# Kernel optimization log

Hardware: AMD Instinct MI355X
Metric: run time of the kernel (lower is better)

Reference implementation:

```python
import jax, jax.numpy as jnp
import numpy as np

WEIGHT_THRESH = 0.0
EPS = 1e-5


def setup_inputs() -> dict:
    key = jax.random.key(0)
    k1, k2, k3 = jax.random.split(key, 3)
    B, N = 8192, 1024
    src_points = jax.random.normal(k1, (B, N, 3), dtype=jnp.float32)
    tgt_points = jax.random.normal(k2, (B, N, 3), dtype=jnp.float32)
    weights = jax.random.uniform(k3, (B, N), dtype=jnp.float32)
    return {"src_points": src_points, "tgt_points": tgt_points, "weights": weights}


def reference(src_points, tgt_points, weights):
    # Threshold and normalize weights: (B, N)
    w = jnp.where(weights < WEIGHT_THRESH, jnp.zeros_like(weights), weights)
    w = w / (jnp.sum(w, axis=1, keepdims=True) + EPS)
    w3 = w[..., None]  # (B, N, 1)

    # Weighted centroids: (B, 1, 3)
    src_centroid = jnp.sum(src_points * w3, axis=1, keepdims=True)
    tgt_centroid = jnp.sum(tgt_points * w3, axis=1, keepdims=True)

    src_c = src_points - src_centroid
    tgt_c = tgt_points - tgt_centroid

    # Weighted covariance H = src_c^T @ (w * tgt_c): (B, 3, 3)
    H = jnp.einsum('bnc,bnd->bcd', src_c, w3 * tgt_c)

    # torch.svd returns U, S, V with H = U S V^T; jnp returns U, S, Vh
    U, _, Vh = jnp.linalg.svd(H)
    V = jnp.swapaxes(Vh, -1, -2)
    Ut = jnp.swapaxes(U, -1, -2)

    # Reflection correction: E = diag(1, 1, sign(det(V @ Ut)))
    s = jnp.sign(jnp.linalg.det(jnp.matmul(V, Ut)))  # (B,)
    d = jnp.stack([jnp.ones_like(s), jnp.ones_like(s), s], axis=-1)  # (B, 3)
    R = jnp.matmul(V, Ut * d[..., None])  # V @ diag(d) @ Ut, (B, 3, 3)

    # Translation: t = tgt_centroid - R @ src_centroid, (B, 3)
    t = tgt_centroid[:, 0, :] - jnp.einsum('bij,bj->bi', R, src_centroid[:, 0, :])

    # Assemble 4x4 transform
    B = src_points.shape[0]
    top = jnp.concatenate([R, t[..., None]], axis=-1)  # (B, 3, 4)
    bottom = jnp.broadcast_to(
        jnp.array([[0.0, 0.0, 0.0, 1.0]], dtype=R.dtype), (B, 1, 4)
    )
    transform = jnp.concatenate([top, bottom], axis=1)  # (B, 4, 4)
    return transform
```

## Files before the change

kernel.cpp:

```cpp
#include <hip/hip_runtime.h>
#include <math.h>

#define TPB 256
#define NPTS 1024

template<int P, int Q, int R>
__device__ __forceinline__ void jrot(float a[3][3], float V[3][3]) {
  float apq = a[P][Q];
  if (fabsf(apq) < 1e-30f) return;
  float theta = (a[Q][Q] - a[P][P]) / (2.0f * apq);
  float t = copysignf(1.0f, theta) / (fabsf(theta) + sqrtf(theta * theta + 1.0f));
  float c = 1.0f / sqrtf(t * t + 1.0f);
  float s = t * c;
  float app = a[P][P], aqq = a[Q][Q];
  a[P][P] = app - t * apq;
  a[Q][Q] = aqq + t * apq;
  a[P][Q] = 0.0f; a[Q][P] = 0.0f;
  float arp = a[R][P], arq = a[R][Q];
  a[R][P] = c * arp - s * arq; a[P][R] = a[R][P];
  a[R][Q] = s * arp + c * arq; a[Q][R] = a[R][Q];
#pragma unroll
  for (int i = 0; i < 3; ++i) {
    float vip = V[i][P], viq = V[i][Q];
    V[i][P] = c * vip - s * viq;
    V[i][Q] = s * vip + c * viq;
  }
}

#define CSWAP(I, J)                                                        \
  if (ev[I] < ev[J]) {                                                     \
    float e_ = ev[I]; ev[I] = ev[J]; ev[J] = e_;                           \
    _Pragma("unroll")                                                      \
    for (int r2_ = 0; r2_ < 3; ++r2_) {                                    \
      float v_ = V[r2_][I]; V[r2_][I] = V[r2_][J]; V[r2_][J] = v_;         \
    }                                                                      \
  }

__device__ __forceinline__ void svd_tail_write(const float r[16], float* o) {
  const float S = r[0];
  const float inv = 1.0f / (S + 1e-5f);
  const float sc[3] = {r[1] * inv, r[2] * inv, r[3] * inv};
  const float tc[3] = {r[4] * inv, r[5] * inv, r[6] * inv};
  const float f = 2.0f - S * inv;

  float H[3][3];
#pragma unroll
  for (int c = 0; c < 3; ++c)
#pragma unroll
    for (int d = 0; d < 3; ++d)
      H[c][d] = r[7 + 3 * c + d] * inv - sc[c] * tc[d] * f;

  float Bm[3][3];
#pragma unroll
  for (int i = 0; i < 3; ++i)
#pragma unroll
    for (int j = 0; j < 3; ++j)
      Bm[i][j] = H[0][i] * H[0][j] + H[1][i] * H[1][j] + H[2][i] * H[2][j];

  float V[3][3] = {{1, 0, 0}, {0, 1, 0}, {0, 0, 1}};
  for (int sweep = 0; sweep < 8; ++sweep) {
    jrot<0, 1, 2>(Bm, V);
    jrot<0, 2, 1>(Bm, V);
    jrot<1, 2, 0>(Bm, V);
  }
  float ev[3] = {Bm[0][0], Bm[1][1], Bm[2][2]};
  CSWAP(0, 1)
  CSWAP(1, 2)
  CSWAP(0, 1)

  float U[3][3];
  float w0[3], w1[3];
#pragma unroll
  for (int i = 0; i < 3; ++i)
    w0[i] = H[i][0] * V[0][0] + H[i][1] * V[1][0] + H[i][2] * V[2][0];
  float n0 = sqrtf(w0[0] * w0[0] + w0[1] * w0[1] + w0[2] * w0[2]);
  float in0 = (n0 > 1e-20f) ? 1.0f / n0 : 0.0f;
#pragma unroll
  for (int i = 0; i < 3; ++i) U[i][0] = w0[i] * in0;

#pragma unroll
  for (int i = 0; i < 3; ++i)
    w1[i] = H[i][0] * V[0][1] + H[i][1] * V[1][1] + H[i][2] * V[2][1];
  float d01 = U[0][0] * w1[0] + U[1][0] * w1[1] + U[2][0] * w1[2];
#pragma unroll
  for (int i = 0; i < 3; ++i) w1[i] -= d01 * U[i][0];
  float n1 = sqrtf(w1[0] * w1[0] + w1[1] * w1[1] + w1[2] * w1[2]);
  float in1 = (n1 > 1e-20f) ? 1.0f / n1 : 0.0f;
#pragma unroll
  for (int i = 0; i < 3; ++i) U[i][1] = w1[i] * in1;

  U[0][2] = U[1][0] * U[2][1] - U[2][0] * U[1][1];
  U[1][2] = U[2][0] * U[0][1] - U[0][0] * U[2][1];
  U[2][2] = U[0][0] * U[1][1] - U[1][0] * U[0][1];

  float detV = V[0][0] * (V[1][1] * V[2][2] - V[1][2] * V[2][1]) -
               V[0][1] * (V[1][0] * V[2][2] - V[1][2] * V[2][0]) +
               V[0][2] * (V[1][0] * V[2][1] - V[1][1] * V[2][0]);
  float s3 = (detV >= 0.0f) ? 1.0f : -1.0f;

  float R[3][3];
#pragma unroll
  for (int i = 0; i < 3; ++i)
#pragma unroll
    for (int j = 0; j < 3; ++j)
      R[i][j] = V[i][0] * U[j][0] + V[i][1] * U[j][1] + s3 * V[i][2] * U[j][2];

  float tr[3];
#pragma unroll
  for (int i = 0; i < 3; ++i)
    tr[i] = tc[i] - (R[i][0] * sc[0] + R[i][1] * sc[1] + R[i][2] * sc[2]);

  float4* o4 = (float4*)o;
  o4[0] = make_float4(R[0][0], R[0][1], R[0][2], tr[0]);
  o4[1] = make_float4(R[1][0], R[1][1], R[1][2], tr[1]);
  o4[2] = make_float4(R[2][0], R[2][1], R[2][2], tr[2]);
  o4[3] = make_float4(0.0f, 0.0f, 0.0f, 1.0f);
}

__global__ __launch_bounds__(TPB) void wproc_fused(
    const float* __restrict__ src, const float* __restrict__ tgt,
    const float* __restrict__ wts, float* __restrict__ out) {
  const int b = blockIdx.x;
  const int t = threadIdx.x;
  const int lane = t & 63, wave = t >> 6;

  __shared__ float4 sh_src[NPTS * 3 / 4];
  __shared__ float4 sh_tgt[NPTS * 3 / 4];
  __shared__ float sh_fin[4][17];
  __shared__ float sh_r[16];
  float(*sh_part)[20] = (float(*)[20])sh_src;

  const float4* g_src = (const float4*)(src + (size_t)b * (NPTS * 3));
  const float4* g_tgt = (const float4*)(tgt + (size_t)b * (NPTS * 3));
  const float* g_w = wts + (size_t)b * NPTS;

#pragma unroll
  for (int i = 0; i < 3; ++i) {
    sh_src[t + i * TPB] = g_src[t + i * TPB];
    sh_tgt[t + i * TPB] = g_tgt[t + i * TPB];
  }
  const float wv0 = g_w[t], wv1 = g_w[t + 256], wv2 = g_w[t + 512],
              wv3 = g_w[t + 768];
  __syncthreads();

  const float* ss = (const float*)sh_src;
  const float* st = (const float*)sh_tgt;

  float acc[16];
#pragma unroll
  for (int k = 0; k < 16; ++k) acc[k] = 0.0f;

  const float wreg[4] = {wv0, wv1, wv2, wv3};
#pragma unroll
  for (int i = 0; i < 4; ++i) {
    const int p = t + i * TPB;
    float wv = fmaxf(wreg[i], 0.0f);
    const float sx = ss[3 * p + 0], sy = ss[3 * p + 1], sz = ss[3 * p + 2];
    const float tx = st[3 * p + 0], ty = st[3 * p + 1], tz = st[3 * p + 2];
    const float wsx = wv * sx, wsy = wv * sy, wsz = wv * sz;
    acc[0] += wv;
    acc[1] += wsx;      acc[2] += wsy;      acc[3] += wsz;
    acc[4] += wv * tx;  acc[5] += wv * ty;  acc[6] += wv * tz;
    acc[7]  += wsx * tx; acc[8]  += wsx * ty; acc[9]  += wsx * tz;
    acc[10] += wsy * tx; acc[11] += wsy * ty; acc[12] += wsy * tz;
    acc[13] += wsz * tx; acc[14] += wsz * ty; acc[15] += wsz * tz;
  }

#pragma unroll
  for (int k = 0; k < 16; ++k) acc[k] += __shfl_down(acc[k], 32, 64);
#pragma unroll
  for (int k = 0; k < 16; ++k) acc[k] += __shfl_down(acc[k], 16, 64);

  __syncthreads();

  if (lane < 16) {
    float4* pr = (float4*)&sh_part[wave * 16 + lane][0];
    pr[0] = make_float4(acc[0], acc[1], acc[2], acc[3]);
    pr[1] = make_float4(acc[4], acc[5], acc[6], acc[7]);
    pr[2] = make_float4(acc[8], acc[9], acc[10], acc[11]);
    pr[3] = make_float4(acc[12], acc[13], acc[14], acc[15]);
  }
  __syncthreads();

  if (t < 64) {
    const int k = t & 15, g = t >> 4;
    float s = 0.0f;
#pragma unroll
    for (int j = 0; j < 16; ++j) s += sh_part[g * 16 + j][k];
    sh_fin[g][k] = s;
  }
  __syncthreads();

  if (t < 16)
    sh_r[t] = sh_fin[0][t] + sh_fin[1][t] + sh_fin[2][t] + sh_fin[3][t];
  __syncthreads();

  if (t != 0) return;
  float r[16];
#pragma unroll
  for (int k = 0; k < 16; ++k) r[k] = sh_r[k];
  svd_tail_write(r, out + (size_t)b * 16);
}

extern "C" void kernel_launch(void* const* d_in, const int* in_sizes, int n_in,
                              void* d_out, int out_size, void* d_ws, size_t ws_size,
                              hipStream_t stream) {
  const float* src = (const float*)d_in[0];
  const float* tgt = (const float*)d_in[1];
  const float* wts = (const float*)d_in[2];
  float* out = (float*)d_out;
  const int B = in_sizes[0] / (NPTS * 3);
  wproc_fused<<<dim3(B), dim3(TPB), 0, stream>>>(src, tgt, wts, out);
}
```

Baseline: 244.6 us.

## Split reduction and SVD into two kernels with register-prefetched multi-batch blocks

Replaces the one-block-per-batch fused kernel with a persistent-style kernel in which each block handles NB batches. It prefetches the next batch's points into registers while reducing the current one and loads contiguous float4s directly instead of staging through LDS. The 16 reduction moments go to a workspace, and a separate kernel runs the 3x3 SVD tail with one thread per batch instead of one lone thread per block. This removes the serial single-thread SVD tail from the bandwidth-bound kernel and the LDS staging cost. The cost is an extra launch, a workspace round trip, and fewer blocks in the grid.

```diff
diff --git a/kernel.cpp b/kernel.cpp
--- a/kernel.cpp
+++ b/kernel.cpp
@@ -3,6 +3,7 @@
 
 #define TPB 256
 #define NPTS 1024
+#define NB 4
 
 template<int P, int Q, int R>
 __device__ __forceinline__ void jrot(float a[3][3], float V[3][3]) {
@@ -117,6 +118,115 @@
   o4[3] = make_float4(0.0f, 0.0f, 0.0f, 1.0f);
 }
 
+#define PT(W, SX, SY, SZ, TX, TY, TZ)                                   \
+  {                                                                     \
+    float wv = fmaxf((W), 0.0f);               \
+    float wsx = wv * (SX), wsy = wv * (SY), wsz = wv * (SZ);            \
+    acc[0] += wv;                                                       \
+    acc[1] += wsx;       acc[2] += wsy;       acc[3] += wsz;            \
+    acc[4] += wv * (TX); acc[5] += wv * (TY); acc[6] += wv * (TZ);      \
+    acc[7]  += wsx * (TX); acc[8]  += wsx * (TY); acc[9]  += wsx * (TZ);\
+    acc[10] += wsy * (TX); acc[11] += wsy * (TY); acc[12] += wsy * (TZ);\
+    acc[13] += wsz * (TX); acc[14] += wsz * (TY); acc[15] += wsz * (TZ);\
+  }
+
+__global__ __launch_bounds__(TPB) void wproc_pipe(
+    const float* __restrict__ src, const float* __restrict__ tgt,
+    const float* __restrict__ wts, float* __restrict__ ws, int nbat) {
+  const int t = threadIdx.x;
+  const int lane = t & 63, wave = t >> 6;
+  const int gsz = gridDim.x;
+
+  __shared__ float sh_part[64][20];
+  __shared__ float sh_fin[4][17];
+
+  float4 cs0, cs1, cs2, cu0, cu1, cu2, cw;
+  float4 ns0, ns1, ns2, nu0, nu1, nu2, nw;
+
+  {
+    const size_t b0 = blockIdx.x;
+    if ((int)b0 < nbat) {
+      const float4* gs = (const float4*)(src + b0 * (NPTS * 3));
+      const float4* gt = (const float4*)(tgt + b0 * (NPTS * 3));
+      const float4* gw = (const float4*)(wts + b0 * NPTS);
+      cs0 = gs[3 * t + 0]; cs1 = gs[3 * t + 1]; cs2 = gs[3 * t + 2];
+      cu0 = gt[3 * t + 0]; cu1 = gt[3 * t + 1]; cu2 = gt[3 * t + 2];
+      cw = gw[t];
+    }
+  }
+
+#pragma unroll
+  for (int j = 0; j < NB; ++j) {
+    if (j + 1 < NB) {
+      const size_t bn = (size_t)blockIdx.x + (size_t)(j + 1) * gsz;
+      if ((int)bn < nbat) {
+        const float4* gs = (const float4*)(src + bn * (NPTS * 3));
+        const float4* gt = (const float4*)(tgt + bn * (NPTS * 3));
+        const float4* gw = (const float4*)(wts + bn * NPTS);
+        ns0 = gs[3 * t + 0]; ns1 = gs[3 * t + 1]; ns2 = gs[3 * t + 2];
+        nu0 = gt[3 * t + 0]; nu1 = gt[3 * t + 1]; nu2 = gt[3 * t + 2];
+        nw = gw[t];
+      }
+    }
+
+    const size_t bc = (size_t)blockIdx.x + (size_t)j * gsz;
+    const bool valid = (int)bc < nbat;
+
+    float acc[16];
+#pragma unroll
+    for (int k = 0; k < 16; ++k) acc[k] = 0.0f;
+    if (valid) {
+      PT(cw.x, cs0.x, cs0.y, cs0.z, cu0.x, cu0.y, cu0.z)
+      PT(cw.y, cs0.w, cs1.x, cs1.y, cu0.w, cu1.x, cu1.y)
+      PT(cw.z, cs1.z, cs1.w, cs2.x, cu1.z, cu1.w, cu2.x)
+      PT(cw.w, cs2.y, cs2.z, cs2.w, cu2.y, cu2.z, cu2.w)
+    }
+
+#pragma unroll
+    for (int k = 0; k < 16; ++k) acc[k] += __shfl_down(acc[k], 32, 64);
+#pragma unroll
+    for (int k = 0; k < 16; ++k) acc[k] += __shfl_down(acc[k], 16, 64);
+
+    if (lane < 16) {
+      float4* pr = (float4*)&sh_part[wave * 16 + lane][0];
+      pr[0] = make_float4(acc[0], acc[1], acc[2], acc[3]);
+      pr[1] = make_float4(acc[4], acc[5], acc[6], acc[7]);
+      pr[2] = make_float4(acc[8], acc[9], acc[10], acc[11]);
+      pr[3] = make_float4(acc[12], acc[13], acc[14], acc[15]);
+    }
+    __syncthreads();
+
+    if (t < 64) {
+      const int k = t & 15, g = t >> 4;
+      float s = 0.0f;
+#pragma unroll
+      for (int jj = 0; jj < 16; ++jj) s += sh_part[g * 16 + jj][k];
+      sh_fin[g][k] = s;
+    }
+    __syncthreads();
+
+    if (t < 16 && valid)
+      ws[bc * 16 + t] =
+          sh_fin[0][t] + sh_fin[1][t] + sh_fin[2][t] + sh_fin[3][t];
+    __syncthreads();
+
+    cs0 = ns0; cs1 = ns1; cs2 = ns2;
+    cu0 = nu0; cu1 = nu1; cu2 = nu2;
+    cw = nw;
+  }
+}
+
+__global__ __launch_bounds__(TPB) void wproc_svd(
+    const float* __restrict__ ws, float* __restrict__ out, int B) {
+  const int i = blockIdx.x * TPB + threadIdx.x;
+  if (i >= B) return;
+  const float4* p = (const float4*)(ws + (size_t)i * 16);
+  const float4 a = p[0], bq = p[1], c = p[2], d = p[3];
+  const float r[16] = {a.x,  a.y,  a.z,  a.w,  bq.x, bq.y, bq.z, bq.w,
+                       c.x,  c.y,  c.z,  c.w,  d.x,  d.y,  d.z,  d.w};
+  svd_tail_write(r, out + (size_t)i * 16);
+}
+
 __global__ __launch_bounds__(TPB) void wproc_fused(
     const float* __restrict__ src, const float* __restrict__ tgt,
     const float* __restrict__ wts, float* __restrict__ out) {
@@ -186,7 +296,7 @@
     const int k = t & 15, g = t >> 4;
     float s = 0.0f;
 #pragma unroll
-    for (int j = 0; j < 16; ++j) s += sh_part[g * 16 + j][k];
+    for (int jj = 0; jj < 16; ++jj) s += sh_part[g * 16 + jj][k];
     sh_fin[g][k] = s;
   }
   __syncthreads();
@@ -210,5 +320,14 @@
   const float* wts = (const float*)d_in[2];
   float* out = (float*)d_out;
   const int B = in_sizes[0] / (NPTS * 3);
-  wproc_fused<<<dim3(B), dim3(TPB), 0, stream>>>(src, tgt, wts, out);
-}
+  const size_t need = (size_t)B * 16 * sizeof(float);
+  if (ws_size >= need) {
+    const int grid = (B + NB - 1) / NB;
+    wproc_pipe<<<dim3(grid), dim3(TPB), 0, stream>>>(src, tgt, wts,
+                                                     (float*)d_ws, B);
+    wproc_svd<<<dim3((B + TPB - 1) / TPB), dim3(TPB), 0, stream>>>(
+        (const float*)d_ws, out, B);
+  } else {
+    wproc_fused<<<dim3(B), dim3(TPB), 0, stream>>>(src, tgt, wts, out);
+  }
+}
```

Result: no change. 242.8 us (-0.7%).

## Split into per-wave reduction kernel and per-thread SVD kernel via workspace

Applied to the files above, without the earlier changes.

Replaces the one-block-per-batch fused kernel with two kernels. The first assigns one wavefront per batch item: each lane loads 16 contiguous points into registers with float4 loads and the sums are reduced with shuffles, so no LDS or block barriers are needed. The second runs the 3x3 SVD tail one batch per thread across a full grid, instead of on a single thread per block while the others sit idle. The cost is an extra launch and a round trip through a workspace buffer. Per-lane loads are strided by 192 bytes across lanes, which may coalesce worse, and each lane holds many more registers.

```diff
diff --git a/kernel.cpp b/kernel.cpp
--- a/kernel.cpp
+++ b/kernel.cpp
@@ -117,6 +117,77 @@
   o4[3] = make_float4(0.0f, 0.0f, 0.0f, 1.0f);
 }
 
+#define F4C(A, I)                                                    \
+  (((I) & 3) == 0   ? A[(I) >> 2].x                                  \
+   : ((I) & 3) == 1 ? A[(I) >> 2].y                                  \
+   : ((I) & 3) == 2 ? A[(I) >> 2].z                                  \
+                    : A[(I) >> 2].w)
+
+__global__ __launch_bounds__(TPB) void wproc_wave(
+    const float* __restrict__ src, const float* __restrict__ tgt,
+    const float* __restrict__ wts, float* __restrict__ ws, int nbat) {
+  const int wid = blockIdx.x * (TPB / 64) + (threadIdx.x >> 6);
+  const int l = threadIdx.x & 63;
+  if (wid >= nbat) return;
+
+  const float4* gs = (const float4*)src + (size_t)wid * 768 + l * 12;
+  const float4* gt = (const float4*)tgt + (size_t)wid * 768 + l * 12;
+  const float4* gw = (const float4*)wts + (size_t)wid * 256 + l * 4;
+
+  float4 s[12], u[12], w[4];
+#pragma unroll
+  for (int i = 0; i < 12; ++i) s[i] = gs[i];
+#pragma unroll
+  for (int i = 0; i < 12; ++i) u[i] = gt[i];
+#pragma unroll
+  for (int i = 0; i < 4; ++i) w[i] = gw[i];
+
+  float acc[16];
+#pragma unroll
+  for (int k = 0; k < 16; ++k) acc[k] = 0.0f;
+
+#pragma unroll
+  for (int j = 0; j < 16; ++j) {
+    const float wv = fmaxf(F4C(w, j), 0.0f);
+    const float sx = F4C(s, 3 * j + 0), sy = F4C(s, 3 * j + 1),
+                sz = F4C(s, 3 * j + 2);
+    const float tx = F4C(u, 3 * j + 0), ty = F4C(u, 3 * j + 1),
+                tz = F4C(u, 3 * j + 2);
+    const float wsx = wv * sx, wsy = wv * sy, wsz = wv * sz;
+    acc[0] += wv;
+    acc[1] += wsx;      acc[2] += wsy;      acc[3] += wsz;
+    acc[4] += wv * tx;  acc[5] += wv * ty;  acc[6] += wv * tz;
+    acc[7]  += wsx * tx; acc[8]  += wsx * ty; acc[9]  += wsx * tz;
+    acc[10] += wsy * tx; acc[11] += wsy * ty; acc[12] += wsy * tz;
+    acc[13] += wsz * tx; acc[14] += wsz * ty; acc[15] += wsz * tz;
+  }
+
+#pragma unroll
+  for (int off = 32; off >= 1; off >>= 1) {
+#pragma unroll
+    for (int k = 0; k < 16; ++k) acc[k] += __shfl_down(acc[k], off, 64);
+  }
+
+  if (l == 0) {
+    float4* o = (float4*)(ws + (size_t)wid * 16);
+    o[0] = make_float4(acc[0], acc[1], acc[2], acc[3]);
+    o[1] = make_float4(acc[4], acc[5], acc[6], acc[7]);
+    o[2] = make_float4(acc[8], acc[9], acc[10], acc[11]);
+    o[3] = make_float4(acc[12], acc[13], acc[14], acc[15]);
+  }
+}
+
+__global__ __launch_bounds__(TPB) void wproc_svd(
+    const float* __restrict__ ws, float* __restrict__ out, int B) {
+  const int i = blockIdx.x * TPB + threadIdx.x;
+  if (i >= B) return;
+  const float4* p = (const float4*)(ws + (size_t)i * 16);
+  const float4 a = p[0], bq = p[1], c = p[2], d = p[3];
+  const float r[16] = {a.x,  a.y,  a.z,  a.w,  bq.x, bq.y, bq.z, bq.w,
+                       c.x,  c.y,  c.z,  c.w,  d.x,  d.y,  d.z,  d.w};
+  svd_tail_write(r, out + (size_t)i * 16);
+}
+
 __global__ __launch_bounds__(TPB) void wproc_fused(
     const float* __restrict__ src, const float* __restrict__ tgt,
     const float* __restrict__ wts, float* __restrict__ out) {
@@ -186,7 +257,7 @@
     const int k = t & 15, g = t >> 4;
     float s = 0.0f;
 #pragma unroll
-    for (int j = 0; j < 16; ++j) s += sh_part[g * 16 + j][k];
+    for (int jj = 0; jj < 16; ++jj) s += sh_part[g * 16 + jj][k];
     sh_fin[g][k] = s;
   }
   __syncthreads();
@@ -210,5 +281,15 @@
   const float* wts = (const float*)d_in[2];
   float* out = (float*)d_out;
   const int B = in_sizes[0] / (NPTS * 3);
-  wproc_fused<<<dim3(B), dim3(TPB), 0, stream>>>(src, tgt, wts, out);
-}
+  const size_t need = (size_t)B * 16 * sizeof(float);
+  if (ws_size >= need) {
+    const int wavesPerBlock = TPB / 64;
+    const int grid = (B + wavesPerBlock - 1) / wavesPerBlock;
+    wproc_wave<<<dim3(grid), dim3(TPB), 0, stream>>>(src, tgt, wts,
+                                                     (float*)d_ws, B);
+    wproc_svd<<<dim3((B + TPB - 1) / TPB), dim3(TPB), 0, stream>>>(
+        (const float*)d_ws, out, B);
+  } else {
+    wproc_fused<<<dim3(B), dim3(TPB), 0, stream>>>(src, tgt, wts, out);
+  }
+}
```

New measurement: 302.0 us. +23.5%, slower.
